# Optimization experiments

Hardware: AMD Instinct MI355X
Metric: run time of the kernel (lower is better)

The kernel has to match this reference:

```python
import jax, jax.numpy as jnp
import numpy as np

CONF_THRES = 0.1
IOU_THRES = 0.6
MAX_DET = 300
MAX_WH = 4096.0  # class offset for non-agnostic NMS
NEG_SLOPE = 0.01  # nn.LeakyReLU default


def xywh2xyxy(p):
    xy, wh = p[..., :2], p[..., 2:4]
    return jnp.concatenate([xy - wh / 2, xy + wh / 2], axis=-1)


def pairwise_iou(a, b):
    area_a = (a[:, 2] - a[:, 0]) * (a[:, 3] - a[:, 1])
    area_b = (b[:, 2] - b[:, 0]) * (b[:, 3] - b[:, 1])
    lt = jnp.maximum(a[:, None, :2], b[None, :, :2])
    rb = jnp.minimum(a[:, None, 2:], b[None, :, 2:])
    wh = jnp.clip(rb - lt, 0.0)
    inter = wh[..., 0] * wh[..., 1]
    return inter / (area_a[:, None] + area_b[None, :] - inter + 1e-7)


def nms_single(pred):  # pred: [N, 5+nc]
    boxes = xywh2xyxy(pred[:, :4])
    scores = pred[:, 5:] * pred[:, 4:5]  # obj * cls
    conf = jnp.max(scores, axis=1)
    cls = jnp.argmax(scores, axis=1)
    conf = jnp.where(conf > CONF_THRES, conf, 0.0)
    topv, topi = jax.lax.top_k(conf, MAX_DET)
    b = boxes[topi]                      # [K,4]
    c = cls[topi]
    valid = topv > CONF_THRES
    bo = b + (c.astype(b.dtype) * MAX_WH)[:, None]  # class-offset boxes
    iou = pairwise_iou(bo, bo)           # [K,K]
    idx = jnp.arange(MAX_DET)
    def body(i, keep):
        sup = keep[i] & (iou[i] > IOU_THRES) & (idx > i)
        return keep & ~sup
    keep = jax.lax.fori_loop(0, MAX_DET, body, valid)
    return b, keep


def bilinear_sample(feat, y, x):  # feat [C,H,W], y/x [K,P] -> [C,K,P]
    C, H, W = feat.shape
    y = jnp.clip(y, 0.0, H - 1.0)
    x = jnp.clip(x, 0.0, W - 1.0)
    y0 = jnp.floor(y).astype(jnp.int32)
    x0 = jnp.floor(x).astype(jnp.int32)
    y1 = jnp.minimum(y0 + 1, H - 1)
    x1 = jnp.minimum(x0 + 1, W - 1)
    ly = y - y0
    lx = x - x0
    return (feat[:, y0, x0] * ((1 - ly) * (1 - lx))
            + feat[:, y0, x1] * ((1 - ly) * lx)
            + feat[:, y1, x0] * (ly * (1 - lx))
            + feat[:, y1, x1] * (ly * lx))


def roi_align_1x1(feat, boxes, scale):  # feat [C,H,W], boxes [K,4] xyxy (input-px)
    b = boxes * scale
    w = jnp.maximum(b[:, 2] - b[:, 0], 1.0)
    h = jnp.maximum(b[:, 3] - b[:, 1], 1.0)
    off = jnp.array([0.5, 1.5], dtype=boxes.dtype)
    xs = b[:, 0:1] + off[None, :] * (w[:, None] / 2.0)  # [K,2]
    ys = b[:, 1:2] + off[None, :] * (h[:, None] / 2.0)
    yy = ys[:, jnp.array([0, 0, 1, 1])]  # [K,4] 2x2 grid
    xx = xs[:, jnp.array([0, 1, 0, 1])]
    v = bilinear_sample(feat, yy, xx)    # [C,K,4]
    return jnp.mean(v, axis=2).T         # [K,C]


def rescale_boxes(bbox, hw, hw0):  # scale_coords + normalize by orig shape
    gain = jnp.minimum(hw[0] / hw0[0], hw[1] / hw0[1])
    pad_x = (hw[1] - hw0[1] * gain) / 2.0
    pad_y = (hw[0] - hw0[0] * gain) / 2.0
    x1 = jnp.clip((bbox[:, 0] - pad_x) / gain, 0.0, hw0[1])
    y1 = jnp.clip((bbox[:, 1] - pad_y) / gain, 0.0, hw0[0])
    x2 = jnp.clip((bbox[:, 2] - pad_x) / gain, 0.0, hw0[1])
    y2 = jnp.clip((bbox[:, 3] - pad_y) / gain, 0.0, hw0[0])
    # divide by shapes[i][0] indexed [w,h,w,h]
    return jnp.stack([x1 / hw0[1], y1 / hw0[0], x2 / hw0[1], y2 / hw0[0]], axis=1)


def setup_inputs() -> dict:
    key = jax.random.key(0)
    ks = jax.random.split(key, 10)
    B, N, NC = 8, 25500, 80
    xy = jax.random.uniform(ks[0], (B, N, 2), minval=0.0, maxval=640.0)
    wh = jax.random.uniform(ks[1], (B, N, 2), minval=8.0, maxval=160.0)
    obj = jax.random.uniform(ks[2], (B, N, 1))
    cls = jax.random.uniform(ks[3], (B, N, NC))
    preds = jnp.concatenate([xy, wh, obj, cls], axis=-1)
    feat1 = jax.random.normal(ks[4], (B, 128, 80, 80), dtype=jnp.float32)
    feat2 = jax.random.normal(ks[5], (B, 256, 40, 40), dtype=jnp.float32)
    feat3 = jax.random.normal(ks[6], (B, 512, 20, 20), dtype=jnp.float32)
    feat4 = jax.random.normal(ks[7], (B, 1024, 10, 10), dtype=jnp.float32)
    orig_hw = jnp.tile(jnp.array([[720.0, 1280.0]], dtype=jnp.float32), (B, 1))
    W1 = jax.random.normal(ks[8], (1920, 256), dtype=jnp.float32) * 0.02
    b1 = jnp.zeros((256,), dtype=jnp.float32)
    W2 = jax.random.normal(ks[9], (256, 256), dtype=jnp.float32) * 0.02
    b2 = jnp.zeros((256,), dtype=jnp.float32)
    return {"preds": preds, "feat1": feat1, "feat2": feat2, "feat3": feat3,
            "feat4": feat4, "orig_hw": orig_hw, "W1": W1, "b1": b1,
            "W2": W2, "b2": b2}


def reference(preds, feat1, feat2, feat3, feat4, orig_hw, W1, b1, W2, b2):
    preds = jax.lax.stop_gradient(preds)  # out.detach() in the original
    hw = jnp.array(feat1.shape[-2:], dtype=preds.dtype) * 8.0  # network input h,w
    boxes, keep = jax.vmap(nms_single)(preds)  # [B,K,4], [B,K]
    f1 = jax.vmap(lambda f, b: roi_align_1x1(f, b, 1.0 / 8))(feat1, boxes)
    f2 = jax.vmap(lambda f, b: roi_align_1x1(f, b, 1.0 / 16))(feat2, boxes)
    f3 = jax.vmap(lambda f, b: roi_align_1x1(f, b, 1.0 / 32))(feat3, boxes)
    f4 = jax.vmap(lambda f, b: roi_align_1x1(f, b, 1.0 / 64))(feat4, boxes)
    f = jnp.concatenate([f1, f2, f3, f4], axis=-1)  # [B,K,1920]
    h = jax.nn.leaky_relu(f @ W1 + b1, NEG_SLOPE)
    h = jax.nn.leaky_relu(h @ W2 + b2, NEG_SLOPE)   # [B,K,256]
    bb = jax.vmap(lambda b, s: rescale_boxes(b, hw, s))(boxes, orig_hw)
    out = jnp.concatenate([bb, h], axis=-1)  # [B,K,260]
    return out * keep[..., None].astype(out.dtype)
```

## Files before the change

kernel.cpp:

```cpp
#include <hip/hip_runtime.h>
#include <hip/hip_bf16.h>
#include <cstdint>
#include <cstddef>

#define NBATCH 8
#define NANCH 25500
#define MAXDET 300
#define NBINS 2048
#define CAP 2048

typedef __bf16 bf16x8 __attribute__((ext_vector_type(8)));
typedef float floatx4 __attribute__((ext_vector_type(4)));
typedef unsigned long long ull;

__device__ __forceinline__ int conf_bin(float v) {
  unsigned bits = __float_as_uint(v);
  int bin = (int)((bits - 0x3D800000u) >> 14);
  return bin > (NBINS - 1) ? (NBINS - 1) : bin;
}

#define CONF_TILE 64
__global__ __launch_bounds__(256) void conf_kernel(const float* __restrict__ preds,
                                                   float* __restrict__ conf,
                                                   int* __restrict__ cls,
                                                   int* __restrict__ ghist,
                                                   int* __restrict__ ctr, int total) {
  if (blockIdx.x < 16) {
    #pragma unroll
    for (int k = 0; k < 4; ++k)
      ghist[blockIdx.x * 1024 + k * 256 + threadIdx.x] = 0;
  }
  if (blockIdx.x == 16 && threadIdx.x == 0) ctr[0] = 0;
  __shared__ float s[CONF_TILE * 85];
  int base = blockIdx.x * CONF_TILE;
  int nA = total - base; if (nA > CONF_TILE) nA = CONF_TILE;
  int n4 = (nA * 85) >> 2;
  const float4* g4 = (const float4*)(preds + (size_t)base * 85);
  float4* s4 = (float4*)s;
  for (int i = threadIdx.x; i < n4; i += 256) s4[i] = g4[i];
  __syncthreads();
  int lane16 = threadIdx.x & 15;
  int sub = threadIdx.x >> 4;
  #pragma unroll
  for (int r = 0; r < 4; ++r) {
    int a = r * 16 + sub;
    if (a < nA) {
      const float* row = s + a * 85;
      float obj = row[4];
      float best = -1.0f; int bc = 0;
      #pragma unroll
      for (int j = 0; j < 5; ++j) {
        int c = lane16 * 5 + j;
        float v = row[5 + c] * obj;
        if (v > best) { best = v; bc = c; }
      }
      #pragma unroll
      for (int m = 1; m < 16; m <<= 1) {
        float ov = __shfl_xor(best, m, 64);
        int   oc = __shfl_xor(bc,   m, 64);
        if (ov > best || (ov == best && oc < bc)) { best = ov; bc = oc; }
      }
      if (lane16 == 0) {
        int idx = base + a;
        conf[idx] = (best > 0.1f) ? best : 0.0f;
        cls[idx] = bc;
      }
    }
  }
}

struct TransArgs {
  const float* src[6];
  __hip_bfloat16* dst[6];
  int C[6], HW[6], tx[6], tpb[6], start[6];
};

__global__ __launch_bounds__(1024) void mid_kernel(TransArgs a,
                                                   const float* __restrict__ conf,
                                                   const float* __restrict__ preds,
                                                   const int* __restrict__ clsg,
                                                   int* __restrict__ ghist,
                                                   int* __restrict__ ctr,
                                                   float* __restrict__ cand_v, int* __restrict__ cand_i,
                                                   float* __restrict__ boxesWs, int* __restrict__ keepWs,
                                                   const float* __restrict__ orig_hw,
                                                   float* __restrict__ out,
                                                   int n_trans_tiles) {
  #pragma clang fp contract(off)
  __shared__ __align__(16) char smem[42496];
  int bid = blockIdx.x;
  int t = threadIdx.y * 32 + threadIdx.x;

  if (bid < 8) {
    int b = bid;
    int*    s_h  = (int*)smem;
    int*    s_ctr= (int*)(smem + 8192);
    ull   (*mask)[5] = (ull(*)[5])smem;
    float*  lv_s = (float*)(smem + 16384);
    int*    li_s = (int*)(smem + 24576);
    float4* bo4  = (float4*)(smem + 32768);
    float (*bxx)[4] = (float(*)[4])(smem + 37568);
    ull* keepw = (ull*)(smem + 42368);
    ull* nzrow = (ull*)(smem + 42408);
    int* shv   = (int*)(smem + 42448);

    if (t < 300) {
      bo4[t] = make_float4(0.0f, 0.0f, 0.0f, 0.0f);
      bxx[t][0] = 0.0f; bxx[t][1] = 0.0f; bxx[t][2] = 0.0f; bxx[t][3] = 0.0f;
    }
    if (t < 5) nzrow[t] = 0ULL;
    if (t == 1) { shv[0] = NBINS; shv[2] = 0; }
    if (t == 0) {
      while (atomicAdd(ctr, 0) < 64) __builtin_amdgcn_s_sleep(8);
      __threadfence();
    }
    __syncthreads();

    int r[8], suf[8], rs[8];
    int w = t >> 6, lane = t & 63;
    if (t < 256) {
      #pragma unroll
      for (int k = 0; k < 8; ++k)
        r[k] = atomicAdd(&ghist[b * NBINS + (w * 8 + k) * 64 + lane], 0);
      int bsum = 0;
      #pragma unroll
      for (int k = 0; k < 8; ++k) {
        int s = r[k];
        #pragma unroll
        for (int d = 1; d < 64; d <<= 1) {
          int o = __shfl_down(s, d, 64);
          if (lane + d < 64) s += o;
        }
        suf[k] = s - r[k];
        rs[k] = __shfl(s, 0, 64);
        bsum += rs[k];
      }
      if (lane == 0) shv[4 + w] = bsum;
    }
    __syncthreads();
    if (t < 256) {
      int p1 = shv[5], p2 = shv[6], p3 = shv[7];
      int total = shv[4] + p1 + p2 + p3;
      int target = total < 300 ? total : 300;
      int RS = (w == 0) ? (p1 + p2 + p3) : (w == 1) ? (p2 + p3) : (w == 2) ? p3 : 0;
      int run = RS;
      #pragma unroll
      for (int k = 7; k >= 0; --k) {
        int Sx = run + suf[k] + r[k];
        int Sx1 = Sx - r[k];
        int bin = (w * 8 + k) * 64 + lane;
        s_h[bin] = Sx;
        s_ctr[bin] = Sx1;
        if (total > 0 && Sx >= target && Sx1 < target) { shv[0] = bin; shv[2] = Sx; }
        run += rs[k];
      }
      if (t == 0) shv[1] = total;
    }
    __syncthreads();
    int T = shv[0];
    int total = shv[1];
    int Kslots = shv[2];
    int nvalid = total < 300 ? total : 300;

    if (t >= nvalid && t < 300) {
      size_t bi = ((size_t)(b * 300 + t)) * 4;
      boxesWs[bi + 0] = 0.0f; boxesWs[bi + 1] = 0.0f;
      boxesWs[bi + 2] = 0.0f; boxesWs[bi + 3] = 0.0f;
    }
    if (t < 5) {
      int n = nvalid - t * 64;
      keepw[t] = (n <= 0) ? 0ULL : (n >= 64 ? ~0ULL : ((1ULL << n) - 1ULL));
    }

    {
      const float4* cf4 = (const float4*)(conf + (size_t)b * NANCH);
      const int N4 = NANCH >> 2;
      float* cv = cand_v + (size_t)b * NANCH;
      int*   ci = cand_i + (size_t)b * NANCH;
      if (total > 0) {
        for (int i4 = t; i4 < N4; i4 += 1024) {
          float4 v4 = cf4[i4];
          int i0 = i4 * 4;
          float vv[4] = {v4.x, v4.y, v4.z, v4.w};
          #pragma unroll
          for (int q = 0; q < 4; ++q) {
            float v = vv[q];
            if (v > 0.1f) {
              int bin = conf_bin(v);
              if (bin >= T) {
                int slot = atomicAdd(&s_ctr[bin], 1);
                if (slot < CAP) { lv_s[slot] = v; li_s[slot] = i0 + q; }
                else            { cv[slot] = v;   ci[slot] = i0 + q;   }
              }
            }
          }
        }
      }
    }
    __syncthreads();

    {
      const float* cv = cand_v + (size_t)b * NANCH;
      const int*   ci = cand_i + (size_t)b * NANCH;
      for (int sIdx = t; sIdx < Kslots; sIdx += 1024) {
        float v; int id;
        if (sIdx < CAP) { v = lv_s[sIdx]; id = li_s[sIdx]; }
        else            { v = cv[sIdx];   id = ci[sIdx];   }
        int bin = conf_bin(v);
        int lo = (bin + 1 < NBINS) ? s_h[bin + 1] : 0;
        int hi = s_h[bin];
        int rank = lo;
        for (int j = lo; j < hi; ++j) {
          float vj; int ij;
          if (j < CAP) { vj = lv_s[j]; ij = li_s[j]; }
          else         { vj = cv[j];   ij = ci[j];   }
          rank += (int)((vj > v) | ((vj == v) & (ij < id)));
        }
        if (rank < 300) {
          const float* p = preds + ((size_t)b * NANCH + id) * 85;
          float cx = p[0], cy = p[1], wq = p[2], hq = p[3];
          float hw2 = wq * 0.5f, hh2 = hq * 0.5f;
          float x1 = cx - hw2, y1 = cy - hh2, x2 = cx + hw2, y2 = cy + hh2;
          bxx[rank][0] = x1; bxx[rank][1] = y1; bxx[rank][2] = x2; bxx[rank][3] = y2;
          size_t bi = ((size_t)(b * 300 + rank)) * 4;
          boxesWs[bi + 0] = x1; boxesWs[bi + 1] = y1;
          boxesWs[bi + 2] = x2; boxesWs[bi + 3] = y2;
          int c = clsg[(size_t)b * NANCH + id];
          float off = (float)c * 4096.0f;
          float4 ob; ob.x = x1 + off; ob.y = y1 + off; ob.z = x2 + off; ob.w = y2 + off;
          bo4[rank] = ob;
        }
      }
    }
    __syncthreads();

    {
      int wv = t >> 6, ln = t & 63;
      if (wv < 10) {
        int w2 = wv >> 1, half = wv & 1;
        int j = w2 * 64 + ln;
        int jc = j < 300 ? j : 0;
        float4 jb = bo4[jc];
        float ja = (jb.z - jb.x) * (jb.w - jb.y);
        bool jv = j < 300;
        int iend = w2 * 64 + 64; if (iend > 300) iend = 300;
        int i0 = half * 150, i1 = i0 + 150; if (i1 > iend) i1 = iend;
        #pragma unroll 4
        for (int i = i0; i < i1; ++i) {
          float4 ib = bo4[i];
          float ai = (ib.z - ib.x) * (ib.w - ib.y);
          float ltx = fmaxf(ib.x, jb.x);
          float lty = fmaxf(ib.y, jb.y);
          float rbx = fminf(ib.z, jb.z);
          float rby = fminf(ib.w, jb.w);
          float wx = fmaxf(rbx - ltx, 0.0f);
          float wy = fmaxf(rby - lty, 0.0f);
          float inter = wx * wy;
          float iou = inter / (ai + ja - inter + 1e-7f);
          ull bal = __ballot(jv && (j > i) && (iou > 0.6f));
          if (ln == 0) {
            mask[i][w2] = bal;
            if (bal) atomicOr(&nzrow[i >> 6], 1ULL << (i & 63));
          }
        }
      }
    }
    __syncthreads();
    if (t == 0) {
      ull kw[5], nz[5];
      #pragma unroll
      for (int w2 = 0; w2 < 5; ++w2) { kw[w2] = keepw[w2]; nz[w2] = nzrow[w2]; }
      #pragma unroll
      for (int w2 = 0; w2 < 5; ++w2) {
        ull p = kw[w2] & nz[w2];
        while (p) {
          int l = __builtin_ctzll(p);
          p &= p - 1;
          int i = w2 * 64 + l;
          for (int w3 = w2; w3 < 5; ++w3) {
            ull m = mask[i][w3];
            kw[w3] &= ~m;
            if (w3 == w2) p &= ~m;
          }
        }
      }
      #pragma unroll
      for (int w2 = 0; w2 < 5; ++w2) keepw[w2] = kw[w2];
    }
    __syncthreads();
    if (t < 300) {
      int kp = (int)((keepw[t >> 6] >> (t & 63)) & 1ULL);
      keepWs[b * 300 + t] = kp;
      float oh = orig_hw[b * 2 + 0], ow = orig_hw[b * 2 + 1];
      float gain = fminf(640.0f / oh, 640.0f / ow);
      float padx = (640.0f - ow * gain) * 0.5f;
      float pady = (640.0f - oh * gain) * 0.5f;
      float x1 = fminf(fmaxf((bxx[t][0] - padx) / gain, 0.0f), ow) / ow;
      float y1 = fminf(fmaxf((bxx[t][1] - pady) / gain, 0.0f), oh) / oh;
      float x2 = fminf(fmaxf((bxx[t][2] - padx) / gain, 0.0f), ow) / ow;
      float y2 = fminf(fmaxf((bxx[t][3] - pady) / gain, 0.0f), oh) / oh;
      size_t o = ((size_t)(b * 300 + t)) * 260;
      out[o + 0] = kp ? x1 : 0.0f;
      out[o + 1] = kp ? y1 : 0.0f;
      out[o + 2] = kp ? x2 : 0.0f;
      out[o + 3] = kp ? y2 : 0.0f;
    }
    return;
  }

  if (bid < 72) {
    int hb = bid - 8;
    int b = hb >> 3, seg = hb & 7;
    int* sh = (int*)smem;
    sh[t] = 0; sh[t + 1024] = 0;
    __syncthreads();
    const int N4 = NANCH >> 2;
    int i0 = (N4 * seg) >> 3, i1 = (N4 * (seg + 1)) >> 3;
    const float4* cf4 = (const float4*)(conf + (size_t)b * NANCH);
    for (int i = i0 + t; i < i1; i += 1024) {
      float4 v = cf4[i];
      if (v.x > 0.1f) atomicAdd(&sh[conf_bin(v.x)], 1);
      if (v.y > 0.1f) atomicAdd(&sh[conf_bin(v.y)], 1);
      if (v.z > 0.1f) atomicAdd(&sh[conf_bin(v.z)], 1);
      if (v.w > 0.1f) atomicAdd(&sh[conf_bin(v.w)], 1);
    }
    __syncthreads();
    {
      int c = sh[t];        if (c) atomicAdd(&ghist[b * NBINS + t], c);
      c     = sh[t + 1024]; if (c) atomicAdd(&ghist[b * NBINS + t + 1024], c);
    }
    __syncthreads();
    if (t == 0) { __threadfence(); atomicAdd(ctr, 1); }
    return;
  }

  {
    int sub = threadIdx.y >> 3;
    int tyl = threadIdx.y & 7, tx = threadIdx.x;
    int gt = (bid - 72) * 4 + sub;
    float (*tile)[33] = (float(*)[33])(smem + sub * 4224);
    int s = 0, local = 0, C = 0, HW = 0, p0 = 0, c0 = 0, bb = 0;
    const float* inb = nullptr;
    __hip_bfloat16* outb = nullptr;
    bool act = gt < n_trans_tiles;
    if (act) {
      #pragma unroll
      for (int i = 1; i < 6; ++i) if (gt >= a.start[i]) s = i;
      local = gt - a.start[s];
      C = a.C[s]; HW = a.HW[s];
      int tx0 = a.tx[s], tpb = a.tpb[s];
      bb = local / tpb;
      int rem = local - bb * tpb;
      p0 = (rem % tx0) * 32;
      c0 = (rem / tx0) * 32;
      inb = a.src[s] + (size_t)bb * C * HW;
      outb = a.dst[s] + (size_t)bb * C * HW;
      #pragma unroll
      for (int k = 0; k < 32; k += 8) {
        int c = c0 + tyl + k, p = p0 + tx;
        if (c < C && p < HW) tile[tyl + k][tx] = inb[(size_t)c * HW + p];
      }
    }
    __syncthreads();
    if (act) {
      #pragma unroll
      for (int k = 0; k < 32; k += 8) {
        int p = p0 + tyl + k, c = c0 + tx;
        if (p < HW && c < C) outb[(size_t)p * C + c] = __float2bfloat16(tile[tx][tyl + k]);
      }
    }
  }
}

__global__ __launch_bounds__(256) void roi_kernel(const float* __restrict__ boxes,
                                                  const __hip_bfloat16* __restrict__ fT1, const __hip_bfloat16* __restrict__ fT2,
                                                  const __hip_bfloat16* __restrict__ fT3, const __hip_bfloat16* __restrict__ fT4,
                                                  __hip_bfloat16* __restrict__ f) {
  int b = blockIdx.x & 7;
  int r = blockIdx.x >> 3;
  __shared__ int t_off[4][16];
  __shared__ float t_w[4][16];
  int t = threadIdx.x;
  const int Hs[4] = {80, 40, 20, 10};
  const int Cs[4] = {128, 256, 512, 1024};
  const float ss[4] = {0.125f, 0.0625f, 0.03125f, 0.015625f};
  size_t bbase = ((size_t)(b * 300 + r)) * 4;
  float bx0 = boxes[bbase + 0];
  float by0 = boxes[bbase + 1];
  float bx1 = boxes[bbase + 2];
  float by1 = boxes[bbase + 3];
  if (t < 64) {
    int lv = t >> 4, k = t & 15, pp = k >> 2, nb = k & 3;
    float s = ss[lv];
    int H = Hs[lv], W = Hs[lv], C = Cs[lv];
    float b0 = bx0 * s, b1 = by0 * s, b2 = bx1 * s, b3 = by1 * s;
    float w = fmaxf(b2 - b0, 1.0f), h = fmaxf(b3 - b1, 1.0f);
    const float offv[2] = {0.5f, 1.5f};
    float px = b0 + offv[pp & 1] * (w * 0.5f);
    float py = b1 + offv[pp >> 1] * (h * 0.5f);
    float y = fminf(fmaxf(py, 0.0f), (float)(H - 1));
    float x = fminf(fmaxf(px, 0.0f), (float)(W - 1));
    int y0 = (int)floorf(y), x0 = (int)floorf(x);
    int y1 = min(y0 + 1, H - 1), x1 = min(x0 + 1, W - 1);
    float ly = y - (float)y0, lx = x - (float)x0;
    int yy = (nb & 2) ? y1 : y0;
    int xx = (nb & 1) ? x1 : x0;
    float wy = (nb & 2) ? ly : (1.0f - ly);
    float wx = (nb & 1) ? lx : (1.0f - lx);
    t_off[lv][k] = (yy * W + xx) * C;
    t_w[lv][k] = wy * wx;
  }
  __syncthreads();
  const __hip_bfloat16* bases[4] = {
    fT1 + (size_t)b * 6400 * 128,
    fT2 + (size_t)b * 1600 * 256,
    fT3 + (size_t)b * 400 * 512,
    fT4 + (size_t)b * 100 * 1024
  };
  __hip_bfloat16* frow = f + (size_t)(b * 300 + r) * 1920;
  int cbase = 0;
  #pragma unroll
  for (int lv = 0; lv < 4; ++lv) {
    int C = Cs[lv];
    const __hip_bfloat16* base = bases[lv];
    for (int c = t; c < C; c += 256) {
      float acc = 0.0f;
      #pragma unroll
      for (int k = 0; k < 16; ++k)
        acc += t_w[lv][k] * __bfloat162float(base[t_off[lv][k] + c]);
      frow[cbase + c] = __float2bfloat16(acc * 0.25f);
    }
    cbase += C;
  }
}

#define GLDS16(gp, lp) __builtin_amdgcn_global_load_lds( \
    (const __attribute__((address_space(1))) unsigned int*)(gp), \
    (__attribute__((address_space(3))) unsigned int*)(lp), 16, 0, 0)

__global__ __launch_bounds__(256) void gemm_tile_kernel(const __hip_bfloat16* __restrict__ A,
                                                        const __hip_bfloat16* __restrict__ BT,
                                                        const float* __restrict__ bias,
                                                        __hip_bfloat16* __restrict__ Cb,
                                                        float* __restrict__ Cf,
                                                        const int* __restrict__ keep,
                                                        int M, int N, int K, int ldc, int coff) {
  __shared__ __hip_bfloat16 sA[2][64 * 64];
  __shared__ __hip_bfloat16 sB[2][64 * 64];
  int tid = threadIdx.x;
  int bm = blockIdx.x * 64, bn = blockIdx.y * 64;
  int wave = tid >> 6, lane = tid & 63;
  int wr = wave >> 1, wc = wave & 1;
  int idx16 = lane & 15, kb = lane >> 4;
  floatx4 acc[2][2] = {};
  int nt = K >> 6;

  auto stage = [&](int buf, int t) {
    int k0 = t << 6;
    #pragma unroll
    for (int i = 0; i < 2; ++i) {
      int c = tid + i * 256;
      int row = c >> 3, cc = c & 7;
      int scc = cc ^ (row & 7);
      GLDS16(A + (size_t)(bm + row) * K + k0 + scc * 8,
             (char*)&sA[buf][0] + c * 16);
    }
    #pragma unroll
    for (int i = 0; i < 2; ++i) {
      int c = tid + i * 256;
      int row = c >> 3, cc = c & 7;
      int scc = cc ^ (row & 7);
      GLDS16(BT + (size_t)(bn + row) * K + k0 + scc * 8,
             (char*)&sB[buf][0] + c * 16);
    }
  };

  stage(0, 0);
  asm volatile("s_waitcnt vmcnt(0)" ::: "memory");
  __syncthreads();
  int cur = 0;
  for (int t = 0; t < nt; ++t) {
    if (t + 1 < nt) stage(cur ^ 1, t + 1);
    const char* Ab = (const char*)&sA[cur][0];
    const char* Bb = (const char*)&sB[cur][0];
    #pragma unroll
    for (int s = 0; s < 2; ++s) {
      bf16x8 af[2], bg[2];
      #pragma unroll
      for (int m = 0; m < 2; ++m) {
        int row = wr * 32 + m * 16 + idx16;
        int chunk = s * 4 + kb;
        af[m] = *(const bf16x8*)(Ab + row * 128 + ((chunk ^ (row & 7)) * 16));
      }
      #pragma unroll
      for (int n = 0; n < 2; ++n) {
        int row = wc * 32 + n * 16 + idx16;
        int chunk = s * 4 + kb;
        bg[n] = *(const bf16x8*)(Bb + row * 128 + ((chunk ^ (row & 7)) * 16));
      }
      #pragma unroll
      for (int m = 0; m < 2; ++m)
        #pragma unroll
        for (int n = 0; n < 2; ++n)
          acc[m][n] = __builtin_amdgcn_mfma_f32_16x16x32_bf16(af[m], bg[n], acc[m][n], 0, 0, 0);
    }
    asm volatile("s_waitcnt vmcnt(0)" ::: "memory");
    __syncthreads();
    cur ^= 1;
  }
  int col = lane & 15, rb4 = (lane >> 4) * 4;
  #pragma unroll
  for (int m = 0; m < 2; ++m) {
    #pragma unroll
    for (int n = 0; n < 2; ++n) {
      #pragma unroll
      for (int r = 0; r < 4; ++r) {
        int orow = bm + wr * 32 + m * 16 + rb4 + r;
        int ocol = bn + wc * 32 + n * 16 + col;
        if (orow >= M) continue;
        float v = acc[m][n][r] + bias[ocol];
        v = (v >= 0.0f) ? v : 0.01f * v;
        if (Cb) Cb[(size_t)orow * N + ocol] = __float2bfloat16(v);
        if (Cf) {
          float km = keep ? (keep[orow] ? 1.0f : 0.0f) : 1.0f;
          Cf[(size_t)orow * ldc + coff + ocol] = v * km;
        }
      }
    }
  }
}

extern "C" void kernel_launch(void* const* d_in, const int* in_sizes, int n_in,
                              void* d_out, int out_size, void* d_ws, size_t ws_size,
                              hipStream_t stream) {
  (void)in_sizes; (void)n_in; (void)out_size; (void)ws_size;
  const float* preds  = (const float*)d_in[0];
  const float* feat1  = (const float*)d_in[1];
  const float* feat2  = (const float*)d_in[2];
  const float* feat3  = (const float*)d_in[3];
  const float* feat4  = (const float*)d_in[4];
  const float* orighw = (const float*)d_in[5];
  const float* W1     = (const float*)d_in[6];
  const float* b1     = (const float*)d_in[7];
  const float* W2     = (const float*)d_in[8];
  const float* b2     = (const float*)d_in[9];
  float* out = (float*)d_out;

  char* ws = (char*)d_ws;
  size_t off = 0;
  auto alloc = [&](size_t bytes) -> void* {
    void* p = ws + off;
    off = (off + bytes + 255) & ~(size_t)255;
    return p;
  };
  const int BN = NBATCH * NANCH;
  float*  conf   = (float*)alloc((size_t)BN * 4);
  int*    cls    = (int*)  alloc((size_t)BN * 4);
  float*  cand_v = (float*)alloc((size_t)BN * 4);
  int*    cand_i = (int*)  alloc((size_t)BN * 4);
  int*    ghist  = (int*)  alloc((size_t)NBATCH * NBINS * 4);
  int*    ctr    = (int*)  alloc(256);
  float*  boxes  = (float*)alloc((size_t)NBATCH * 300 * 4 * 4);
  int*    keep   = (int*)  alloc((size_t)NBATCH * 300 * 4);
  __hip_bfloat16* fT1  = (__hip_bfloat16*)alloc((size_t)NBATCH * 6400 * 128 * 2);
  __hip_bfloat16* fT2  = (__hip_bfloat16*)alloc((size_t)NBATCH * 1600 * 256 * 2);
  __hip_bfloat16* fT3  = (__hip_bfloat16*)alloc((size_t)NBATCH * 400 * 512 * 2);
  __hip_bfloat16* fT4  = (__hip_bfloat16*)alloc((size_t)NBATCH * 100 * 1024 * 2);
  __hip_bfloat16* fmat = (__hip_bfloat16*)alloc((size_t)2400 * 1920 * 2);
  __hip_bfloat16* h1b  = (__hip_bfloat16*)alloc((size_t)2400 * 256 * 2);
  __hip_bfloat16* W1T  = (__hip_bfloat16*)alloc((size_t)256 * 1920 * 2);
  __hip_bfloat16* W2T  = (__hip_bfloat16*)alloc((size_t)256 * 256 * 2);

  conf_kernel<<<(BN + CONF_TILE - 1) / CONF_TILE, 256, 0, stream>>>(preds, conf, cls, ghist, ctr, BN);

  TransArgs ta;
  ta.src[0] = feat1; ta.dst[0] = fT1; ta.C[0] = 128;  ta.HW[0] = 6400; ta.tx[0] = 200;
  ta.src[1] = feat2; ta.dst[1] = fT2; ta.C[1] = 256;  ta.HW[1] = 1600; ta.tx[1] = 50;
  ta.src[2] = feat3; ta.dst[2] = fT3; ta.C[2] = 512;  ta.HW[2] = 400;  ta.tx[2] = 13;
  ta.src[3] = feat4; ta.dst[3] = fT4; ta.C[3] = 1024; ta.HW[3] = 100;  ta.tx[3] = 4;
  ta.src[4] = W1;    ta.dst[4] = W1T; ta.C[4] = 1920; ta.HW[4] = 256;  ta.tx[4] = 8;
  ta.src[5] = W2;    ta.dst[5] = W2T; ta.C[5] = 256;  ta.HW[5] = 256;  ta.tx[5] = 8;
  int n_tiles = 0;
  for (int s = 0; s < 6; ++s) {
    int ty = (ta.C[s] + 31) / 32;
    int nbatch = (s < 4) ? NBATCH : 1;
    ta.tpb[s] = ta.tx[s] * ty;
    ta.start[s] = n_tiles;
    n_tiles += ta.tpb[s] * nbatch;
  }
  int mid_grid = 72 + (n_tiles + 3) / 4;
  mid_kernel<<<mid_grid, dim3(32, 32), 0, stream>>>(ta, conf, preds, cls, ghist, ctr,
                                                    cand_v, cand_i, boxes, keep, orighw, out,
                                                    n_tiles);

  roi_kernel<<<2400, 256, 0, stream>>>(boxes, fT1, fT2, fT3, fT4, fmat);
  gemm_tile_kernel<<<dim3(38, 4), 256, 0, stream>>>(fmat, W1T, b1, h1b, nullptr, nullptr,
                                                    2400, 256, 1920, 0, 0);
  gemm_tile_kernel<<<dim3(38, 4), 256, 0, stream>>>(h1b, W2T, b2, nullptr, out, keep,
                                                    2400, 256, 256, 260, 4);
}
```

Baseline: 118.5 us.

## Compute per-batch histogram in-block and use persistent wave-level transpose tiles

The global histogram built by 64 separate blocks, with its spin-wait on an atomic counter, is replaced by each of the 8 NMS blocks building its own conf histogram in shared memory. This removes the ghist/ctr global atomics, the zeroing in conf_kernel, and the cross-block dependency. The transpose part becomes a fixed grid of 432 persistent blocks where each wave loops over 32x32 tiles using float4 loads and a padded shared tile. The trade-off is that each NMS block now reads its 25500 conf values twice serially, and shared memory grows to 68 KB per block, which may lower occupancy.

After: 121.0 us. 1.02x slower.

```diff
diff --git a/kernel.cpp b/kernel.cpp
--- a/kernel.cpp
+++ b/kernel.cpp
@@ -22,15 +22,7 @@
 #define CONF_TILE 64
 __global__ __launch_bounds__(256) void conf_kernel(const float* __restrict__ preds,
                                                    float* __restrict__ conf,
-                                                   int* __restrict__ cls,
-                                                   int* __restrict__ ghist,
-                                                   int* __restrict__ ctr, int total) {
-  if (blockIdx.x < 16) {
-    #pragma unroll
-    for (int k = 0; k < 4; ++k)
-      ghist[blockIdx.x * 1024 + k * 256 + threadIdx.x] = 0;
-  }
-  if (blockIdx.x == 16 && threadIdx.x == 0) ctr[0] = 0;
+                                                   int* __restrict__ cls, int total) {
   __shared__ float s[CONF_TILE * 85];
   int base = blockIdx.x * CONF_TILE;
   int nA = total - base; if (nA > CONF_TILE) nA = CONF_TILE;
@@ -79,296 +71,296 @@
                                                    const float* __restrict__ conf,
                                                    const float* __restrict__ preds,
                                                    const int* __restrict__ clsg,
-                                                   int* __restrict__ ghist,
-                                                   int* __restrict__ ctr,
                                                    float* __restrict__ cand_v, int* __restrict__ cand_i,
                                                    float* __restrict__ boxesWs, int* __restrict__ keepWs,
                                                    const float* __restrict__ orig_hw,
                                                    float* __restrict__ out,
                                                    int n_trans_tiles) {
   #pragma clang fp contract(off)
-  __shared__ __align__(16) char smem[42496];
+  __shared__ __align__(16) char smem[69632];
   int bid = blockIdx.x;
   int t = threadIdx.y * 32 + threadIdx.x;
 
-  if (bid < 8) {
-    int b = bid;
-    int*    s_h  = (int*)smem;
-    int*    s_ctr= (int*)(smem + 8192);
-    ull   (*mask)[5] = (ull(*)[5])smem;
-    float*  lv_s = (float*)(smem + 16384);
-    int*    li_s = (int*)(smem + 24576);
-    float4* bo4  = (float4*)(smem + 32768);
-    float (*bxx)[4] = (float(*)[4])(smem + 37568);
-    ull* keepw = (ull*)(smem + 42368);
-    ull* nzrow = (ull*)(smem + 42408);
-    int* shv   = (int*)(smem + 42448);
-
-    if (t < 300) {
-      bo4[t] = make_float4(0.0f, 0.0f, 0.0f, 0.0f);
-      bxx[t][0] = 0.0f; bxx[t][1] = 0.0f; bxx[t][2] = 0.0f; bxx[t][3] = 0.0f;
-    }
-    if (t < 5) nzrow[t] = 0ULL;
-    if (t == 1) { shv[0] = NBINS; shv[2] = 0; }
-    if (t == 0) {
-      while (atomicAdd(ctr, 0) < 64) __builtin_amdgcn_s_sleep(8);
-      __threadfence();
-    }
-    __syncthreads();
-
-    int r[8], suf[8], rs[8];
-    int w = t >> 6, lane = t & 63;
-    if (t < 256) {
-      #pragma unroll
-      for (int k = 0; k < 8; ++k)
-        r[k] = atomicAdd(&ghist[b * NBINS + (w * 8 + k) * 64 + lane], 0);
-      int bsum = 0;
-      #pragma unroll
-      for (int k = 0; k < 8; ++k) {
-        int s = r[k];
+  if (bid >= 8) {
+    int wv = t >> 6, l = t & 63;
+    int wid = (bid - 8) * 16 + wv;
+    int wtot = ((int)gridDim.x - 8) * 16;
+    float* tile = (float*)(smem + wv * 4352);
+    for (int gt = wid; gt < n_trans_tiles; gt += wtot) {
+      int s = 0;
+      #pragma unroll
+      for (int i = 1; i < 6; ++i) if (gt >= a.start[i]) s = i;
+      int local = gt - a.start[s];
+      int C = a.C[s], HW = a.HW[s], tx0 = a.tx[s], tpb = a.tpb[s];
+      int bb = local / tpb;
+      int rem = local - bb * tpb;
+      int p0 = (rem % tx0) * 32;
+      int c0 = (rem / tx0) * 32;
+      const float* inb = a.src[s] + (size_t)bb * C * HW;
+      __hip_bfloat16* outb = a.dst[s] + (size_t)bb * C * HW;
+      if (p0 + 32 <= HW) {
         #pragma unroll
-        for (int d = 1; d < 64; d <<= 1) {
-          int o = __shfl_down(s, d, 64);
-          if (lane + d < 64) s += o;
-        }
-        suf[k] = s - r[k];
-        rs[k] = __shfl(s, 0, 64);
-        bsum += rs[k];
-      }
-      if (lane == 0) shv[4 + w] = bsum;
-    }
-    __syncthreads();
-    if (t < 256) {
-      int p1 = shv[5], p2 = shv[6], p3 = shv[7];
-      int total = shv[4] + p1 + p2 + p3;
-      int target = total < 300 ? total : 300;
-      int RS = (w == 0) ? (p1 + p2 + p3) : (w == 1) ? (p2 + p3) : (w == 2) ? p3 : 0;
-      int run = RS;
-      #pragma unroll
-      for (int k = 7; k >= 0; --k) {
-        int Sx = run + suf[k] + r[k];
-        int Sx1 = Sx - r[k];
-        int bin = (w * 8 + k) * 64 + lane;
-        s_h[bin] = Sx;
-        s_ctr[bin] = Sx1;
-        if (total > 0 && Sx >= target && Sx1 < target) { shv[0] = bin; shv[2] = Sx; }
-        run += rs[k];
-      }
-      if (t == 0) shv[1] = total;
-    }
-    __syncthreads();
-    int T = shv[0];
-    int total = shv[1];
-    int Kslots = shv[2];
-    int nvalid = total < 300 ? total : 300;
-
-    if (t >= nvalid && t < 300) {
-      size_t bi = ((size_t)(b * 300 + t)) * 4;
-      boxesWs[bi + 0] = 0.0f; boxesWs[bi + 1] = 0.0f;
-      boxesWs[bi + 2] = 0.0f; boxesWs[bi + 3] = 0.0f;
-    }
-    if (t < 5) {
-      int n = nvalid - t * 64;
-      keepw[t] = (n <= 0) ? 0ULL : (n >= 64 ? ~0ULL : ((1ULL << n) - 1ULL));
-    }
-
-    {
-      const float4* cf4 = (const float4*)(conf + (size_t)b * NANCH);
-      const int N4 = NANCH >> 2;
-      float* cv = cand_v + (size_t)b * NANCH;
-      int*   ci = cand_i + (size_t)b * NANCH;
-      if (total > 0) {
-        for (int i4 = t; i4 < N4; i4 += 1024) {
-          float4 v4 = cf4[i4];
-          int i0 = i4 * 4;
-          float vv[4] = {v4.x, v4.y, v4.z, v4.w};
+        for (int k = 0; k < 4; ++k) {
+          int cr = k * 8 + (l >> 3);
+          int pr = (l & 7) * 4;
+          float4 v = *(const float4*)(inb + (size_t)(c0 + cr) * HW + p0 + pr);
+          float* d = tile + cr * 33 + pr;
+          d[0] = v.x; d[1] = v.y; d[2] = v.z; d[3] = v.w;
+        }
+        asm volatile("s_waitcnt lgkmcnt(0)" ::: "memory");
+        __builtin_amdgcn_sched_barrier(0);
+        #pragma unroll
+        for (int k = 0; k < 16; ++k) {
+          int pr = k * 2 + (l >> 5);
+          int cr = l & 31;
+          outb[(size_t)(p0 + pr) * C + c0 + cr] = __float2bfloat16(tile[cr * 33 + pr]);
+        }
+      } else {
+        int nvp = HW - p0;
+        #pragma unroll
+        for (int k = 0; k < 4; ++k) {
+          int cr = k * 8 + (l >> 3);
+          int pr = (l & 7) * 4;
+          const float* src = inb + (size_t)(c0 + cr) * HW + p0;
+          float* d = tile + cr * 33 + pr;
           #pragma unroll
-          for (int q = 0; q < 4; ++q) {
-            float v = vv[q];
-            if (v > 0.1f) {
-              int bin = conf_bin(v);
-              if (bin >= T) {
-                int slot = atomicAdd(&s_ctr[bin], 1);
-                if (slot < CAP) { lv_s[slot] = v; li_s[slot] = i0 + q; }
-                else            { cv[slot] = v;   ci[slot] = i0 + q;   }
-              }
+          for (int j = 0; j < 4; ++j) d[j] = (pr + j < nvp) ? src[pr + j] : 0.0f;
+        }
+        asm volatile("s_waitcnt lgkmcnt(0)" ::: "memory");
+        __builtin_amdgcn_sched_barrier(0);
+        #pragma unroll
+        for (int k = 0; k < 16; ++k) {
+          int pr = k * 2 + (l >> 5);
+          int cr = l & 31;
+          if (pr < nvp) outb[(size_t)(p0 + pr) * C + c0 + cr] = __float2bfloat16(tile[cr * 33 + pr]);
+        }
+      }
+    }
+    return;
+  }
+
+  int b = bid;
+  int*    s_h  = (int*)smem;
+  int*    s_ctr= (int*)(smem + 8192);
+  ull   (*mask)[5] = (ull(*)[5])smem;
+  float*  lv_s = (float*)(smem + 16384);
+  int*    li_s = (int*)(smem + 24576);
+  float4* bo4  = (float4*)(smem + 32768);
+  float (*bxx)[4] = (float(*)[4])(smem + 37568);
+  ull* keepw = (ull*)(smem + 42368);
+  ull* nzrow = (ull*)(smem + 42408);
+  int* shv   = (int*)(smem + 42448);
+
+  s_h[t] = 0; s_h[t + 1024] = 0;
+  if (t < 300) {
+    bo4[t] = make_float4(0.0f, 0.0f, 0.0f, 0.0f);
+    bxx[t][0] = 0.0f; bxx[t][1] = 0.0f; bxx[t][2] = 0.0f; bxx[t][3] = 0.0f;
+  }
+  if (t < 5) nzrow[t] = 0ULL;
+  if (t == 1) { shv[0] = NBINS; shv[2] = 0; }
+  __syncthreads();
+
+  {
+    const float4* cf4 = (const float4*)(conf + (size_t)b * NANCH);
+    const int N4 = NANCH >> 2;
+    for (int i = t; i < N4; i += 1024) {
+      float4 v = cf4[i];
+      if (v.x > 0.1f) atomicAdd(&s_h[conf_bin(v.x)], 1);
+      if (v.y > 0.1f) atomicAdd(&s_h[conf_bin(v.y)], 1);
+      if (v.z > 0.1f) atomicAdd(&s_h[conf_bin(v.z)], 1);
+      if (v.w > 0.1f) atomicAdd(&s_h[conf_bin(v.w)], 1);
+    }
+  }
+  __syncthreads();
+
+  int r[8], suf[8], rs[8];
+  int w = t >> 6, lane = t & 63;
+  if (t < 256) {
+    #pragma unroll
+    for (int k = 0; k < 8; ++k)
+      r[k] = s_h[(w * 8 + k) * 64 + lane];
+    int bsum = 0;
+    #pragma unroll
+    for (int k = 0; k < 8; ++k) {
+      int s = r[k];
+      #pragma unroll
+      for (int d = 1; d < 64; d <<= 1) {
+        int o = __shfl_down(s, d, 64);
+        if (lane + d < 64) s += o;
+      }
+      suf[k] = s - r[k];
+      rs[k] = __shfl(s, 0, 64);
+      bsum += rs[k];
+    }
+    if (lane == 0) shv[4 + w] = bsum;
+  }
+  __syncthreads();
+  if (t < 256) {
+    int p1 = shv[5], p2 = shv[6], p3 = shv[7];
+    int total = shv[4] + p1 + p2 + p3;
+    int target = total < 300 ? total : 300;
+    int RS = (w == 0) ? (p1 + p2 + p3) : (w == 1) ? (p2 + p3) : (w == 2) ? p3 : 0;
+    int run = RS;
+    #pragma unroll
+    for (int k = 7; k >= 0; --k) {
+      int Sx = run + suf[k] + r[k];
+      int Sx1 = Sx - r[k];
+      int bin = (w * 8 + k) * 64 + lane;
+      s_h[bin] = Sx;
+      s_ctr[bin] = Sx1;
+      if (total > 0 && Sx >= target && Sx1 < target) { shv[0] = bin; shv[2] = Sx; }
+      run += rs[k];
+    }
+    if (t == 0) shv[1] = total;
+  }
+  __syncthreads();
+  int T = shv[0];
+  int total = shv[1];
+  int Kslots = shv[2];
+  int nvalid = total < 300 ? total : 300;
+
+  if (t >= nvalid && t < 300) {
+    size_t bi = ((size_t)(b * 300 + t)) * 4;
+    boxesWs[bi + 0] = 0.0f; boxesWs[bi + 1] = 0.0f;
+    boxesWs[bi + 2] = 0.0f; boxesWs[bi + 3] = 0.0f;
+  }
+  if (t < 5) {
+    int n = nvalid - t * 64;
+    keepw[t] = (n <= 0) ? 0ULL : (n >= 64 ? ~0ULL : ((1ULL << n) - 1ULL));
+  }
+
+  {
+    const float4* cf4 = (const float4*)(conf + (size_t)b * NANCH);
+    const int N4 = NANCH >> 2;
+    float* cv = cand_v + (size_t)b * NANCH;
+    int*   ci = cand_i + (size_t)b * NANCH;
+    if (total > 0) {
+      for (int i4 = t; i4 < N4; i4 += 1024) {
+        float4 v4 = cf4[i4];
+        int i0 = i4 * 4;
+        float vv[4] = {v4.x, v4.y, v4.z, v4.w};
+        #pragma unroll
+        for (int q = 0; q < 4; ++q) {
+          float v = vv[q];
+          if (v > 0.1f) {
+            int bin = conf_bin(v);
+            if (bin >= T) {
+              int slot = atomicAdd(&s_ctr[bin], 1);
+              if (slot < CAP) { lv_s[slot] = v; li_s[slot] = i0 + q; }
+              else            { cv[slot] = v;   ci[slot] = i0 + q;   }
             }
           }
         }
       }
     }
-    __syncthreads();
-
-    {
-      const float* cv = cand_v + (size_t)b * NANCH;
-      const int*   ci = cand_i + (size_t)b * NANCH;
-      for (int sIdx = t; sIdx < Kslots; sIdx += 1024) {
-        float v; int id;
-        if (sIdx < CAP) { v = lv_s[sIdx]; id = li_s[sIdx]; }
-        else            { v = cv[sIdx];   id = ci[sIdx];   }
-        int bin = conf_bin(v);
-        int lo = (bin + 1 < NBINS) ? s_h[bin + 1] : 0;
-        int hi = s_h[bin];
-        int rank = lo;
-        for (int j = lo; j < hi; ++j) {
-          float vj; int ij;
-          if (j < CAP) { vj = lv_s[j]; ij = li_s[j]; }
-          else         { vj = cv[j];   ij = ci[j];   }
-          rank += (int)((vj > v) | ((vj == v) & (ij < id)));
-        }
-        if (rank < 300) {
-          const float* p = preds + ((size_t)b * NANCH + id) * 85;
-          float cx = p[0], cy = p[1], wq = p[2], hq = p[3];
-          float hw2 = wq * 0.5f, hh2 = hq * 0.5f;
-          float x1 = cx - hw2, y1 = cy - hh2, x2 = cx + hw2, y2 = cy + hh2;
-          bxx[rank][0] = x1; bxx[rank][1] = y1; bxx[rank][2] = x2; bxx[rank][3] = y2;
-          size_t bi = ((size_t)(b * 300 + rank)) * 4;
-          boxesWs[bi + 0] = x1; boxesWs[bi + 1] = y1;
-          boxesWs[bi + 2] = x2; boxesWs[bi + 3] = y2;
-          int c = clsg[(size_t)b * NANCH + id];
-          float off = (float)c * 4096.0f;
-          float4 ob; ob.x = x1 + off; ob.y = y1 + off; ob.z = x2 + off; ob.w = y2 + off;
-          bo4[rank] = ob;
-        }
-      }
-    }
-    __syncthreads();
-
-    {
-      int wv = t >> 6, ln = t & 63;
-      if (wv < 10) {
-        int w2 = wv >> 1, half = wv & 1;
-        int j = w2 * 64 + ln;
-        int jc = j < 300 ? j : 0;
-        float4 jb = bo4[jc];
-        float ja = (jb.z - jb.x) * (jb.w - jb.y);
-        bool jv = j < 300;
-        int iend = w2 * 64 + 64; if (iend > 300) iend = 300;
-        int i0 = half * 150, i1 = i0 + 150; if (i1 > iend) i1 = iend;
-        #pragma unroll 4
-        for (int i = i0; i < i1; ++i) {
-          float4 ib = bo4[i];
-          float ai = (ib.z - ib.x) * (ib.w - ib.y);
-          float ltx = fmaxf(ib.x, jb.x);
-          float lty = fmaxf(ib.y, jb.y);
-          float rbx = fminf(ib.z, jb.z);
-          float rby = fminf(ib.w, jb.w);
-          float wx = fmaxf(rbx - ltx, 0.0f);
-          float wy = fmaxf(rby - lty, 0.0f);
-          float inter = wx * wy;
-          float iou = inter / (ai + ja - inter + 1e-7f);
-          ull bal = __ballot(jv && (j > i) && (iou > 0.6f));
-          if (ln == 0) {
-            mask[i][w2] = bal;
-            if (bal) atomicOr(&nzrow[i >> 6], 1ULL << (i & 63));
-          }
-        }
-      }
-    }
-    __syncthreads();
-    if (t == 0) {
-      ull kw[5], nz[5];
-      #pragma unroll
-      for (int w2 = 0; w2 < 5; ++w2) { kw[w2] = keepw[w2]; nz[w2] = nzrow[w2]; }
-      #pragma unroll
-      for (int w2 = 0; w2 < 5; ++w2) {
-        ull p = kw[w2] & nz[w2];
-        while (p) {
-          int l = __builtin_ctzll(p);
-          p &= p - 1;
-          int i = w2 * 64 + l;
-          for (int w3 = w2; w3 < 5; ++w3) {
-            ull m = mask[i][w3];
-            kw[w3] &= ~m;
-            if (w3 == w2) p &= ~m;
-          }
-        }
-      }
-      #pragma unroll
-      for (int w2 = 0; w2 < 5; ++w2) keepw[w2] = kw[w2];
-    }
-    __syncthreads();
-    if (t < 300) {
-      int kp = (int)((keepw[t >> 6] >> (t & 63)) & 1ULL);
-      keepWs[b * 300 + t] = kp;
-      float oh = orig_hw[b * 2 + 0], ow = orig_hw[b * 2 + 1];
-      float gain = fminf(640.0f / oh, 640.0f / ow);
-      float padx = (640.0f - ow * gain) * 0.5f;
-      float pady = (640.0f - oh * gain) * 0.5f;
-      float x1 = fminf(fmaxf((bxx[t][0] - padx) / gain, 0.0f), ow) / ow;
-      float y1 = fminf(fmaxf((bxx[t][1] - pady) / gain, 0.0f), oh) / oh;
-      float x2 = fminf(fmaxf((bxx[t][2] - padx) / gain, 0.0f), ow) / ow;
-      float y2 = fminf(fmaxf((bxx[t][3] - pady) / gain, 0.0f), oh) / oh;
-      size_t o = ((size_t)(b * 300 + t)) * 260;
-      out[o + 0] = kp ? x1 : 0.0f;
-      out[o + 1] = kp ? y1 : 0.0f;
-      out[o + 2] = kp ? x2 : 0.0f;
-      out[o + 3] = kp ? y2 : 0.0f;
-    }
-    return;
-  }
-
-  if (bid < 72) {
-    int hb = bid - 8;
-    int b = hb >> 3, seg = hb & 7;
-    int* sh = (int*)smem;
-    sh[t] = 0; sh[t + 1024] = 0;
-    __syncthreads();
-    const int N4 = NANCH >> 2;
-    int i0 = (N4 * seg) >> 3, i1 = (N4 * (seg + 1)) >> 3;
-    const float4* cf4 = (const float4*)(conf + (size_t)b * NANCH);
-    for (int i = i0 + t; i < i1; i += 1024) {
-      float4 v = cf4[i];
-      if (v.x > 0.1f) atomicAdd(&sh[conf_bin(v.x)], 1);
-      if (v.y > 0.1f) atomicAdd(&sh[conf_bin(v.y)], 1);
-      if (v.z > 0.1f) atomicAdd(&sh[conf_bin(v.z)], 1);
-      if (v.w > 0.1f) atomicAdd(&sh[conf_bin(v.w)], 1);
-    }
-    __syncthreads();
-    {
-      int c = sh[t];        if (c) atomicAdd(&ghist[b * NBINS + t], c);
-      c     = sh[t + 1024]; if (c) atomicAdd(&ghist[b * NBINS + t + 1024], c);
-    }
-    __syncthreads();
-    if (t == 0) { __threadfence(); atomicAdd(ctr, 1); }
-    return;
-  }
+  }
+  __syncthreads();
 
   {
-    int sub = threadIdx.y >> 3;
-    int tyl = threadIdx.y & 7, tx = threadIdx.x;
-    int gt = (bid - 72) * 4 + sub;
-    float (*tile)[33] = (float(*)[33])(smem + sub * 4224);
-    int s = 0, local = 0, C = 0, HW = 0, p0 = 0, c0 = 0, bb = 0;
-    const float* inb = nullptr;
-    __hip_bfloat16* outb = nullptr;
-    bool act = gt < n_trans_tiles;
-    if (act) {
-      #pragma unroll
-      for (int i = 1; i < 6; ++i) if (gt >= a.start[i]) s = i;
-      local = gt - a.start[s];
-      C = a.C[s]; HW = a.HW[s];
-      int tx0 = a.tx[s], tpb = a.tpb[s];
-      bb = local / tpb;
-      int rem = local - bb * tpb;
-      p0 = (rem % tx0) * 32;
-      c0 = (rem / tx0) * 32;
-      inb = a.src[s] + (size_t)bb * C * HW;
-      outb = a.dst[s] + (size_t)bb * C * HW;
-      #pragma unroll
-      for (int k = 0; k < 32; k += 8) {
-        int c = c0 + tyl + k, p = p0 + tx;
-        if (c < C && p < HW) tile[tyl + k][tx] = inb[(size_t)c * HW + p];
-      }
-    }
-    __syncthreads();
-    if (act) {
-      #pragma unroll
-      for (int k = 0; k < 32; k += 8) {
-        int p = p0 + tyl + k, c = c0 + tx;
-        if (p < HW && c < C) outb[(size_t)p * C + c] = __float2bfloat16(tile[tx][tyl + k]);
-      }
-    }
+    const float* cv = cand_v + (size_t)b * NANCH;
+    const int*   ci = cand_i + (size_t)b * NANCH;
+    for (int sIdx = t; sIdx < Kslots; sIdx += 1024) {
+      float v; int id;
+      if (sIdx < CAP) { v = lv_s[sIdx]; id = li_s[sIdx]; }
+      else            { v = cv[sIdx];   id = ci[sIdx];   }
+      int bin = conf_bin(v);
+      int lo = (bin + 1 < NBINS) ? s_h[bin + 1] : 0;
+      int hi = s_h[bin];
+      int rank = lo;
+      for (int j = lo; j < hi; ++j) {
+        float vj; int ij;
+        if (j < CAP) { vj = lv_s[j]; ij = li_s[j]; }
+        else         { vj = cv[j];   ij = ci[j];   }
+        rank += (int)((vj > v) | ((vj == v) & (ij < id)));
+      }
+      if (rank < 300) {
+        const float* p = preds + ((size_t)b * NANCH + id) * 85;
+        float cx = p[0], cy = p[1], wq = p[2], hq = p[3];
+        float hw2 = wq * 0.5f, hh2 = hq * 0.5f;
+        float x1 = cx - hw2, y1 = cy - hh2, x2 = cx + hw2, y2 = cy + hh2;
+        bxx[rank][0] = x1; bxx[rank][1] = y1; bxx[rank][2] = x2; bxx[rank][3] = y2;
+        size_t bi = ((size_t)(b * 300 + rank)) * 4;
+        boxesWs[bi + 0] = x1; boxesWs[bi + 1] = y1;
+        boxesWs[bi + 2] = x2; boxesWs[bi + 3] = y2;
+        int c = clsg[(size_t)b * NANCH + id];
+        float off = (float)c * 4096.0f;
+        float4 ob; ob.x = x1 + off; ob.y = y1 + off; ob.z = x2 + off; ob.w = y2 + off;
+        bo4[rank] = ob;
+      }
+    }
+  }
+  __syncthreads();
+
+  {
+    int wv2 = t >> 6, ln = t & 63;
+    if (wv2 < 10) {
+      int w2 = wv2 >> 1, half = wv2 & 1;
+      int j = w2 * 64 + ln;
+      int jc = j < 300 ? j : 0;
+      float4 jb = bo4[jc];
+      float ja = (jb.z - jb.x) * (jb.w - jb.y);
+      bool jv = j < 300;
+      int iend = w2 * 64 + 64; if (iend > 300) iend = 300;
+      int i0 = half * 150, i1 = i0 + 150; if (i1 > iend) i1 = iend;
+      #pragma unroll 4
+      for (int i = i0; i < i1; ++i) {
+        float4 ib = bo4[i];
+        float ai = (ib.z - ib.x) * (ib.w - ib.y);
+        float ltx = fmaxf(ib.x, jb.x);
+        float lty = fmaxf(ib.y, jb.y);
+        float rbx = fminf(ib.z, jb.z);
+        float rby = fminf(ib.w, jb.w);
+        float wx = fmaxf(rbx - ltx, 0.0f);
+        float wy = fmaxf(rby - lty, 0.0f);
+        float inter = wx * wy;
+        float iou = inter / (ai + ja - inter + 1e-7f);
+        ull bal = __ballot(jv && (j > i) && (iou > 0.6f));
+        if (ln == 0) {
+          mask[i][w2] = bal;
+          if (bal) atomicOr(&nzrow[i >> 6], 1ULL << (i & 63));
+        }
+      }
+    }
+  }
+  __syncthreads();
+  if (t == 0) {
+    ull kw[5], nz[5];
+    #pragma unroll
+    for (int w2 = 0; w2 < 5; ++w2) { kw[w2] = keepw[w2]; nz[w2] = nzrow[w2]; }
+    #pragma unroll
+    for (int w2 = 0; w2 < 5; ++w2) {
+      ull p = kw[w2] & nz[w2];
+      while (p) {
+        int l2 = __builtin_ctzll(p);
+        p &= p - 1;
+        int i = w2 * 64 + l2;
+        for (int w3 = w2; w3 < 5; ++w3) {
+          ull m = mask[i][w3];
+          kw[w3] &= ~m;
+          if (w3 == w2) p &= ~m;
+        }
+      }
+    }
+    #pragma unroll
+    for (int w2 = 0; w2 < 5; ++w2) keepw[w2] = kw[w2];
+  }
+  __syncthreads();
+  if (t < 300) {
+    int kp = (int)((keepw[t >> 6] >> (t & 63)) & 1ULL);
+    keepWs[b * 300 + t] = kp;
+    float oh = orig_hw[b * 2 + 0], ow = orig_hw[b * 2 + 1];
+    float gain = fminf(640.0f / oh, 640.0f / ow);
+    float padx = (640.0f - ow * gain) * 0.5f;
+    float pady = (640.0f - oh * gain) * 0.5f;
+    float x1 = fminf(fmaxf((bxx[t][0] - padx) / gain, 0.0f), ow) / ow;
+    float y1 = fminf(fmaxf((bxx[t][1] - pady) / gain, 0.0f), oh) / oh;
+    float x2 = fminf(fmaxf((bxx[t][2] - padx) / gain, 0.0f), ow) / ow;
+    float y2 = fminf(fmaxf((bxx[t][3] - pady) / gain, 0.0f), oh) / oh;
+    size_t o = ((size_t)(b * 300 + t)) * 260;
+    out[o + 0] = kp ? x1 : 0.0f;
+    out[o + 1] = kp ? y1 : 0.0f;
+    out[o + 2] = kp ? x2 : 0.0f;
+    out[o + 3] = kp ? y2 : 0.0f;
   }
 }
 
@@ -558,8 +550,6 @@
   int*    cls    = (int*)  alloc((size_t)BN * 4);
   float*  cand_v = (float*)alloc((size_t)BN * 4);
   int*    cand_i = (int*)  alloc((size_t)BN * 4);
-  int*    ghist  = (int*)  alloc((size_t)NBATCH * NBINS * 4);
-  int*    ctr    = (int*)  alloc(256);
   float*  boxes  = (float*)alloc((size_t)NBATCH * 300 * 4 * 4);
   int*    keep   = (int*)  alloc((size_t)NBATCH * 300 * 4);
   __hip_bfloat16* fT1  = (__hip_bfloat16*)alloc((size_t)NBATCH * 6400 * 128 * 2);
@@ -571,7 +561,7 @@
   __hip_bfloat16* W1T  = (__hip_bfloat16*)alloc((size_t)256 * 1920 * 2);
   __hip_bfloat16* W2T  = (__hip_bfloat16*)alloc((size_t)256 * 256 * 2);
 
-  conf_kernel<<<(BN + CONF_TILE - 1) / CONF_TILE, 256, 0, stream>>>(preds, conf, cls, ghist, ctr, BN);
+  conf_kernel<<<(BN + CONF_TILE - 1) / CONF_TILE, 256, 0, stream>>>(preds, conf, cls, BN);
 
   TransArgs ta;
   ta.src[0] = feat1; ta.dst[0] = fT1; ta.C[0] = 128;  ta.HW[0] = 6400; ta.tx[0] = 200;
@@ -588,10 +578,9 @@
     ta.start[s] = n_tiles;
     n_tiles += ta.tpb[s] * nbatch;
   }
-  int mid_grid = 72 + (n_tiles + 3) / 4;
-  mid_kernel<<<mid_grid, dim3(32, 32), 0, stream>>>(ta, conf, preds, cls, ghist, ctr,
-                                                    cand_v, cand_i, boxes, keep, orighw, out,
-                                                    n_tiles);
+  mid_kernel<<<8 + 432, dim3(32, 32), 0, stream>>>(ta, conf, preds, cls,
+                                                   cand_v, cand_i, boxes, keep, orighw, out,
+                                                   n_tiles);
 
   roi_kernel<<<2400, 256, 0, stream>>>(boxes, fT1, fT2, fT3, fT4, fmat);
   gemm_tile_kernel<<<dim3(38, 4), 256, 0, stream>>>(fmat, W1T, b1, h1b, nullptr, nullptr,
```
